# Optimization experiments

Measured on AMD Instinct MI355X. Metric: run time of the kernel, lower is better.

The kernel has to match this reference:

```python
import jax, jax.numpy as jnp
import numpy as np

N = 8192
H = 256
E = N * 32
ALPHA = 0.2  # LeakyReLU negative slope from init kwarg alpha


def setup_inputs() -> dict:
    key = jax.random.key(0)
    ks = jax.random.split(key, 8)
    s = 1.0 / np.sqrt(H)
    return {
        "features": jax.random.normal(ks[0], (N, H), jnp.float32),
        "edge_index": jax.random.randint(ks[1], (2, E), 0, N, jnp.int64),
        "W_att": jax.random.normal(ks[2], (H, H), jnp.float32) * s,
        "a_src": jax.random.normal(ks[3], (H,), jnp.float32) * s,
        "a_dst": jax.random.normal(ks[4], (H,), jnp.float32) * s,
        "gcn_w": jax.random.normal(ks[5], (H, H), jnp.float32) * s,
        "gcn_b": jnp.zeros((H,), jnp.float32),
        "out_w": jax.random.normal(ks[6], (H, 2), jnp.float32) * s,
        "out_b": jnp.zeros((2,), jnp.float32),
    }


def reference(features, edge_index, W_att, a_src, a_dst, gcn_w, gcn_b, out_w, out_b):
    n = features.shape[0]
    # --- SingleNodeAttentionLayer (GAT-style dense self-attention, concat=True) ---
    Wh = features @ W_att                       # [N, H]
    e = jax.nn.leaky_relu(
        (Wh @ a_src)[:, None] + (Wh @ a_dst)[None, :], negative_slope=ALPHA
    )                                            # [N, N]
    attn = jax.nn.softmax(e, axis=-1)
    h1 = jax.nn.elu(attn @ Wh)                   # [N, H]
    # --- GCNConv: symmetric-normalized aggregation with self-loops ---
    loops = jnp.arange(n, dtype=edge_index.dtype)
    row = jnp.concatenate([edge_index[0], loops])  # destination
    col = jnp.concatenate([edge_index[1], loops])  # source
    deg = jax.ops.segment_sum(jnp.ones_like(row, dtype=h1.dtype), row, num_segments=n)
    dinv = jax.lax.rsqrt(jnp.maximum(deg, 1e-12))
    norm = dinv[row] * dinv[col]                 # [E+N]
    x = h1 @ gcn_w                               # [N, H]
    agg = jax.ops.segment_sum(x[col] * norm[:, None], row, num_segments=n) + gcn_b
    # --- head: linear -> mean over nodes -> softmax ---
    res = agg @ out_w + out_b                    # [N, 2]
    res = jnp.mean(res, axis=0, keepdims=True)   # [1, 2]
    return jax.nn.softmax(res, axis=-1)
```

## Files before the change

kernel.cpp:

```cpp
#include <hip/hip_runtime.h>
#include <hip/hip_bf16.h>

#define NN 8192
#define HH 256
#define EE (NN*32)
#define ALPHAC 0.2f
#define CHUNK 16
#define NCHUNK (NN/CHUNK)
#define CSPAD 1024

typedef __bf16 bf16x8 __attribute__((ext_vector_type(8)));
typedef float  f32x4  __attribute__((ext_vector_type(4)));

#define OFF_WH     0
#define OFF_S      (OFF_WH + NN*HH)
#define OFF_D      (OFF_S + NN)
#define OFF_SORTD  (OFF_D + NN)
#define OFF_PERM   (OFF_SORTD + NN)
#define OFF_EA     (OFF_PERM + NN)
#define OFF_E1     (OFF_EA + NN)
#define OFF_SAREL  (OFF_E1 + NN)
#define OFF_SBREL  (OFF_SAREL + NN)
#define OFF_ABPART (OFF_SBREL + NN)
#define OFF_CPAB   (OFF_ABPART + 2*NN*HH)
#define OFF_CSA    (OFF_CPAB + 2*(NCHUNK+1)*HH)
#define OFF_CSB    (OFF_CSA + CSPAD)
#define OFF_DEG    (OFF_CSB + CSPAD)
#define OFF_V      (OFF_DEG + NN)
#define OFF_DINV   (OFF_V + HH)
#define OFF_WNODE  (OFF_DINV + NN)
#define OFF_KEYS   (OFF_WNODE + NN)
#define OFF_FB16   (OFF_KEYS + 2*NN)
#define OFF_WT16   (OFF_FB16 + NN*HH/2)
#define OFF_CNT    (OFF_WT16 + HH*HH/2)
#define OFF_WAS    (OFF_CNT + 16)
#define OFF_WAD    (OFF_WAS + HH)

__device__ __forceinline__ float elu1(float x) {
    return x > 0.f ? x : (expf(x) - 1.f);
}

__global__ __launch_bounds__(256) void k_prep(const float* __restrict__ features,
                                              const float* __restrict__ W_att,
                                              const float* __restrict__ a_src,
                                              const float* __restrict__ a_dst,
                                              float* ws) {
    int bid = blockIdx.x, tid = threadIdx.x;
    int wave = tid >> 6, lane = tid & 63;
    if (bid < 1024) {
        int base = (bid*256 + tid)*8;
        float4 a = *(const float4*)(features + base);
        float4 b = *(const float4*)(features + base + 4);
        bf16x8 v;
        v[0]=(__bf16)a.x; v[1]=(__bf16)a.y; v[2]=(__bf16)a.z; v[3]=(__bf16)a.w;
        v[4]=(__bf16)b.x; v[5]=(__bf16)b.y; v[6]=(__bf16)b.z; v[7]=(__bf16)b.w;
        *(bf16x8*)((__bf16*)(ws + OFF_FB16) + base) = v;
    } else if (bid < 1056) {
        int idx0 = ((bid-1024)*256 + tid)*8;
        __bf16* WT = (__bf16*)(ws + OFF_WT16);
        #pragma unroll
        for (int q = 0; q < 8; ++q) {
            int idx = idx0 + q;
            int n = idx >> 8, k = idx & 255;
            WT[idx] = (__bf16)W_att[(size_t)k*HH + n];
        }
    } else if (bid < 1120) {
        int k = (bid - 1056)*4 + wave;
        float4 w = *(const float4*)(W_att + (size_t)k*HH + lane*4);
        float4 as = *(const float4*)(a_src + lane*4);
        float4 ad = *(const float4*)(a_dst + lane*4);
        float ss = w.x*as.x + w.y*as.y + w.z*as.z + w.w*as.w;
        float dd = w.x*ad.x + w.y*ad.y + w.z*ad.z + w.w*ad.w;
        #pragma unroll
        for (int off = 32; off; off >>= 1) {
            ss += __shfl_xor(ss, off);
            dd += __shfl_xor(dd, off);
        }
        if (lane == 0) {
            ws[OFF_WAS + k] = ss;
            ws[OFF_WAD + k] = dd;
        }
    } else {
        int z0 = ((bid-1120)*256 + tid);
        if (z0 < NN + HH) ws[OFF_DEG + z0] = 0.f;
        if (bid == 1120 && tid < 16) ((unsigned*)(ws + OFF_CNT))[tid] = 0u;
    }
}

__global__ __launch_bounds__(256) void k_gemm_deg_sd(const float* __restrict__ features,
                                                     const int* __restrict__ ei, float* ws) {
    int bid = blockIdx.x, tid = threadIdx.x;
    int wave = tid >> 6, lane = tid & 63;
    if (bid < 512) {
        int mt = bid >> 2, nt = bid & 3;
        int ml = lane & 15, quad = lane >> 4;
        int row0 = mt*64 + wave*16;
        int n0 = nt*64;
        const __bf16* FB = (const __bf16*)(ws + OFF_FB16);
        const __bf16* WT = (const __bf16*)(ws + OFF_WT16);
        const __bf16* Ap = FB + (size_t)(row0 + ml)*HH + quad*8;
        const __bf16* B0 = WT + (size_t)(n0 +  0 + ml)*HH + quad*8;
        const __bf16* B1 = WT + (size_t)(n0 + 16 + ml)*HH + quad*8;
        const __bf16* B2 = WT + (size_t)(n0 + 32 + ml)*HH + quad*8;
        const __bf16* B3 = WT + (size_t)(n0 + 48 + ml)*HH + quad*8;
        f32x4 ac0 = {0.f,0.f,0.f,0.f}, ac1 = ac0, ac2 = ac0, ac3 = ac0;
        #pragma unroll
        for (int k0 = 0; k0 < HH; k0 += 32) {
            bf16x8 af = *(const bf16x8*)(Ap + k0);
            ac0 = __builtin_amdgcn_mfma_f32_16x16x32_bf16(af, *(const bf16x8*)(B0 + k0), ac0, 0, 0, 0);
            ac1 = __builtin_amdgcn_mfma_f32_16x16x32_bf16(af, *(const bf16x8*)(B1 + k0), ac1, 0, 0, 0);
            ac2 = __builtin_amdgcn_mfma_f32_16x16x32_bf16(af, *(const bf16x8*)(B2 + k0), ac2, 0, 0, 0);
            ac3 = __builtin_amdgcn_mfma_f32_16x16x32_bf16(af, *(const bf16x8*)(B3 + k0), ac3, 0, 0, 0);
        }
        float* Whp = ws + OFF_WH;
        #pragma unroll
        for (int r = 0; r < 4; ++r) {
            size_t grow = (size_t)(row0 + quad*4 + r)*HH + n0 + ml;
            Whp[grow +  0] = ac0[r];
            Whp[grow + 16] = ac1[r];
            Whp[grow + 32] = ac2[r];
            Whp[grow + 48] = ac3[r];
        }
    } else {
        int b = bid - 512;
        int e = b*512 + tid;
        atomicAdd(ws + OFF_DEG + ei[e], 1.0f);
        atomicAdd(ws + OFF_DEG + ei[e + 256], 1.0f);
        float4 as = *(const float4*)(ws + OFF_WAS + lane*4);
        float4 ad = *(const float4*)(ws + OFF_WAD + lane*4);
        int row0 = b*16 + wave*4;
        #pragma unroll
        for (int r = 0; r < 4; ++r) {
            int row = row0 + r;
            float4 f = *(const float4*)(features + (size_t)row*HH + lane*4);
            float ss = f.x*as.x + f.y*as.y + f.z*as.z + f.w*as.w;
            float dd = f.x*ad.x + f.y*ad.y + f.z*ad.z + f.w*ad.w;
            #pragma unroll
            for (int off = 32; off; off >>= 1) {
                ss += __shfl_xor(ss, off);
                dd += __shfl_xor(dd, off);
            }
            if (lane == 0) {
                ws[OFF_S+row] = ss; ws[OFF_D+row] = dd;
                unsigned u = __float_as_uint(dd);
                unsigned mono = u ^ ((u & 0x80000000u) ? 0xFFFFFFFFu : 0x80000000u);
                ((unsigned long long*)(ws + OFF_KEYS))[row] =
                    (((unsigned long long)mono) << 13) | (unsigned)row;
            }
        }
    }
}

__global__ __launch_bounds__(256) void k_rank_dinv(float* ws) {
    __shared__ unsigned long long lk[NN];
    int bid = blockIdx.x, tid = threadIdx.x;
    int wave = tid >> 6, lane = tid & 63;
    if (bid < 512) {
        const unsigned long long* keys = (const unsigned long long*)(ws + OFF_KEYS);
        for (int m = tid; m < NN/2; m += 256)
            *(ulonglong2*)&lk[m*2] = *(const ulonglong2*)&keys[m*2];
        __syncthreads();
        int jb = bid*16 + wave*4;
        unsigned long long kj0 = lk[jb+0], kj1 = lk[jb+1];
        unsigned long long kj2 = lk[jb+2], kj3 = lk[jb+3];
        int c0 = 0, c1 = 0, c2 = 0, c3 = 0;
        #pragma unroll 4
        for (int it = 0; it < 64; ++it) {
            ulonglong2 kq = *(const ulonglong2*)&lk[(it*64 + lane)*2];
            c0 += (kq.x < kj0); c1 += (kq.x < kj1);
            c2 += (kq.x < kj2); c3 += (kq.x < kj3);
            c0 += (kq.y < kj0); c1 += (kq.y < kj1);
            c2 += (kq.y < kj2); c3 += (kq.y < kj3);
        }
        #pragma unroll
        for (int off = 1; off < 64; off <<= 1) {
            c0 += __shfl_xor(c0, off);
            c1 += __shfl_xor(c1, off);
            c2 += __shfl_xor(c2, off);
            c3 += __shfl_xor(c3, off);
        }
        if (lane == 0) {
            unsigned long long kk[4] = {kj0, kj1, kj2, kj3};
            int cr[4] = {c0, c1, c2, c3};
            #pragma unroll
            for (int q = 0; q < 4; ++q) {
                unsigned long long kv = kk[q];
                int r = cr[q];
                unsigned mm = (unsigned)(kv >> 13);
                unsigned u = (mm & 0x80000000u) ? (mm ^ 0x80000000u) : ~mm;
                float dj = __uint_as_float(u);
                int j = (int)(kv & 8191ULL);
                ws[OFF_SORTD + r] = dj;
                ((int*)ws)[OFF_PERM + r] = j;
                ws[OFF_EA + r] = expf(ALPHAC * dj);
                ws[OFF_E1 + r] = expf(dj);
            }
        }
    } else {
        int i = (bid - 512)*256 + tid;
        float dv = rsqrtf(ws[OFF_DEG + i] + 1.0f);
        ws[OFF_DINV + i] = dv;
        ws[OFF_WNODE + i] = dv*dv;
    }
}

__global__ __launch_bounds__(256) void k_wnode_vecpref(const int* __restrict__ ei, float* ws) {
    int bid = blockIdx.x, tid = threadIdx.x;
    if (bid < NCHUNK) {
        __shared__ int   sp[CHUNK];
        __shared__ float sea[CHUNK], se1[CHUNK];
        int c = bid, h = tid;
        int k0 = c * CHUNK;
        if (h < CHUNK) {
            sp[h]  = ((int*)ws)[OFF_PERM + k0 + h];
            sea[h] = ws[OFF_EA + k0 + h];
            se1[h] = ws[OFF_E1 + k0 + h];
        }
        __syncthreads();
        if (tid < 64) {
            int lane = tid;
            float v = 0.f;
            if (lane < 16) v = sea[lane];
            else if (lane < 32) v = se1[lane-16];
            #pragma unroll
            for (int off = 1; off < 16; off <<= 1) {
                float x = __shfl_up(v, off);
                if ((lane & 15) >= off) v += x;
            }
            if (lane < 16) {
                ws[OFF_SAREL + k0 + lane] = v;
                if (lane == 15) ws[OFF_CSA + c + 1] = v;
            } else if (lane < 32) {
                ws[OFF_SBREL + k0 + lane - 16] = v;
                if (lane == 31) ws[OFF_CSB + c + 1] = v;
            }
        }
        const float* Wh = ws + OFF_WH;
        float wv[CHUNK];
        #pragma unroll
        for (int kk = 0; kk < CHUNK; ++kk)
            wv[kk] = Wh[(size_t)sp[kk]*HH + h];
        float2* abp = (float2*)(ws + OFF_ABPART);
        float acca = 0.f, accb = 0.f;
        #pragma unroll
        for (int kk = 0; kk < CHUNK; ++kk) {
            acca += sea[kk]*wv[kk]; accb += se1[kk]*wv[kk];
            abp[(size_t)(k0+kk)*HH + h] = make_float2(acca, accb);
        }
        float2* cp = (float2*)(ws + OFF_CPAB);
        cp[(size_t)(c+1)*HH + h] = make_float2(acca, accb);
    } else {
        int e = (bid - NCHUNK)*512 + tid;
        int r0 = ei[e],       c0i = ei[EE + e];
        int r1 = ei[e + 256], c1i = ei[EE + e + 256];
        atomicAdd(ws + OFF_WNODE + c0i, ws[OFF_DINV + r0] * ws[OFF_DINV + c0i]);
        atomicAdd(ws + OFF_WNODE + c1i, ws[OFF_DINV + r1] * ws[OFF_DINV + c1i]);
    }
}

__global__ __launch_bounds__(256) void k_chunkscan(float* ws) {
    int bid = blockIdx.x, tid = threadIdx.x;
    if (bid < 32) {
        int h = bid*8 + (tid >> 5);
        int t = tid & 31;
        float2* cp = (float2*)(ws + OFF_CPAB);
        float la[16], lb[16];
        float ta = 0.f, tb = 0.f;
        #pragma unroll
        for (int m = 0; m < 16; ++m) {
            float2 v = cp[(size_t)(t*16 + m + 1)*HH + h];
            la[m] = v.x; lb[m] = v.y;
            ta += la[m]; tb += lb[m];
        }
        float ia = ta, ib = tb;
        #pragma unroll
        for (int off = 1; off < 32; off <<= 1) {
            float xa = __shfl_up(ia, off, 32);
            float xb = __shfl_up(ib, off, 32);
            if (t >= off) { ia += xa; ib += xb; }
        }
        float ba = ia - ta, bb = ib - tb;
        #pragma unroll
        for (int m = 0; m < 16; ++m) {
            cp[(size_t)(t*16 + m)*HH + h] = make_float2(ba, bb);
            ba += la[m]; bb += lb[m];
        }
        if (t == 31) cp[(size_t)NCHUNK*HH + h] = make_float2(ba, bb);
    } else {
        int lane = tid & 63, wvi = tid >> 6;
        bool act = wvi < 2;
        float* cs = ws + (wvi == 1 ? OFF_CSB : OFF_CSA);
        float la[8];
        float ta = 0.f;
        if (act) {
            #pragma unroll
            for (int m = 0; m < 8; ++m) { la[m] = cs[lane*8 + m + 1]; ta += la[m]; }
        }
        float ia = ta;
        #pragma unroll
        for (int off = 1; off < 64; off <<= 1) {
            float x = __shfl_up(ia, off);
            if (lane >= off) ia += x;
        }
        float ba = ia - ta;
        __syncthreads();
        if (act) {
            #pragma unroll
            for (int m = 0; m < 8; ++m) { cs[lane*8 + m] = ba; ba += la[m]; }
            if (lane == 63) cs[NCHUNK] = ba;
        }
    }
}

__global__ __launch_bounds__(256) void k_rows_final(
        const float* __restrict__ gcn_w, const float* __restrict__ gcn_b,
        const float* __restrict__ out_w, const float* __restrict__ out_b,
        float* ws, float* out) {
    __shared__ float sd[NN];
    __shared__ float red[4][256];
    __shared__ float fin[768];
    __shared__ int islast;
    int tid = threadIdx.x;
    for (int m = tid; m < NN/4; m += 256)
        *(float4*)&sd[m*4] = *(const float4*)(ws + OFF_SORTD + m*4);
    __syncthreads();
    int wave = tid >> 6, lane = tid & 63;
    int gw = blockIdx.x*4 + wave;
    const float2* abp  = (const float2*)(ws + OFF_ABPART);
    const float2* cpab = (const float2*)(ws + OFF_CPAB);
    float btot = ws[OFF_CSB + NCHUNK];
    const float4* btr = (const float4*)(cpab + (size_t)NCHUNK*HH);
    float4 bt0 = btr[lane*2], bt1 = btr[lane*2+1];
    float BTx = bt0.y, BTy = bt0.w, BTz = bt1.y, BTw = bt1.w;

    int myr = lane & 3;
    float si_m = ws[OFF_S + gw*4 + myr];
    float tt = -si_m;
    int lo = 0, hi = NN;
    while (lo < hi) {
        int mid = (lo + hi) >> 1;
        if (sd[mid] <= tt) lo = mid + 1; else hi = mid;
    }

    float accx = 0.f, accy = 0.f, accz = 0.f, accw = 0.f;
    #pragma unroll
    for (int r = 0; r < 4; ++r) {
        int i = gw*4 + r;
        int k = __shfl(lo, r);
        float si = __shfl(si_m, r);
        float eas = expf(ALPHAC * si), es = expf(si);
        float av = 0.f, bv = 0.f;
        float Ax=0.f, Ay=0.f, Az=0.f, Aw=0.f, Bx=0.f, By=0.f, Bz=0.f, Bw=0.f;
        if (k > 0) {
            int km = k - 1, cc = km >> 4;
            av = ws[OFF_CSA + cc] + ws[OFF_SAREL + km];
            bv = ws[OFF_CSB + cc] + ws[OFF_SBREL + km];
            const float4* pr = (const float4*)(abp + (size_t)km*HH);
            const float4* cr = (const float4*)(cpab + (size_t)cc*HH);
            float4 p0 = pr[lane*2], p1 = pr[lane*2+1];
            float4 q0 = cr[lane*2], q1 = cr[lane*2+1];
            Ax = p0.x + q0.x; Bx = p0.y + q0.y;
            Ay = p0.z + q0.z; By = p0.w + q0.w;
            Az = p1.x + q1.x; Bz = p1.y + q1.y;
            Aw = p1.z + q1.z; Bw = p1.w + q1.w;
        }
        float Z = eas*av + es*(btot - bv);
        float invZ = 1.f / Z;
        float w = ws[OFF_WNODE + i];
        accx += w * elu1((eas*Ax + es*(BTx - Bx)) * invZ);
        accy += w * elu1((eas*Ay + es*(BTy - By)) * invZ);
        accz += w * elu1((eas*Az + es*(BTz - Bz)) * invZ);
        accw += w * elu1((eas*Aw + es*(BTw - Bw)) * invZ);
    }
    red[wave][lane*4+0] = accx;
    red[wave][lane*4+1] = accy;
    red[wave][lane*4+2] = accz;
    red[wave][lane*4+3] = accw;
    __syncthreads();
    float sum = red[0][tid] + red[1][tid] + red[2][tid] + red[3][tid];
    atomicAdd(ws + OFF_V + tid, sum);

    __syncthreads();
    if (tid == 0) {
        unsigned* cnt = (unsigned*)(ws + OFF_CNT);
        unsigned arrived = __hip_atomic_fetch_add(&cnt[0], 1u,
                               __ATOMIC_ACQ_REL, __HIP_MEMORY_SCOPE_AGENT) + 1u;
        islast = (arrived == 512u);
    }
    __syncthreads();
    if (islast) {
        float* vl  = fin;
        float* r0s = fin + 256;
        float* r1s = fin + 512;
        int t = tid;
        vl[t] = __hip_atomic_load(ws + OFF_V + t, __ATOMIC_RELAXED,
                                  __HIP_MEMORY_SCOPE_AGENT);
        __syncthreads();
        float acc = 0.f;
        for (int h = 0; h < HH; ++h) acc += vl[h] * gcn_w[(size_t)h*HH + t];
        float meanv = acc * (1.0f/(float)NN) + gcn_b[t];
        r0s[t] = meanv * out_w[t*2+0];
        r1s[t] = meanv * out_w[t*2+1];
        __syncthreads();
        for (int off = 128; off; off >>= 1) {
            if (t < off) { r0s[t] += r0s[t+off]; r1s[t] += r1s[t+off]; }
            __syncthreads();
        }
        if (t == 0) {
            float res0 = r0s[0] + out_b[0], res1 = r1s[0] + out_b[1];
            float m = fmaxf(res0, res1);
            float e0 = expf(res0 - m), e1v = expf(res1 - m);
            float inv = 1.f / (e0 + e1v);
            out[0] = e0 * inv;
            out[1] = e1v * inv;
        }
    }
}

extern "C" void kernel_launch(void* const* d_in, const int* in_sizes, int n_in,
                              void* d_out, int out_size, void* d_ws, size_t ws_size,
                              hipStream_t stream) {
    const float* features = (const float*)d_in[0];
    const int*   eidx     = (const int*)d_in[1];
    const float* W_att    = (const float*)d_in[2];
    const float* a_src    = (const float*)d_in[3];
    const float* a_dst    = (const float*)d_in[4];
    const float* gcn_w    = (const float*)d_in[5];
    const float* gcn_b    = (const float*)d_in[6];
    const float* out_w    = (const float*)d_in[7];
    const float* out_b    = (const float*)d_in[8];
    float* ws  = (float*)d_ws;
    float* out = (float*)d_out;

    k_prep<<<1154, 256, 0, stream>>>(features, W_att, a_src, a_dst, ws);
    k_gemm_deg_sd<<<1024, 256, 0, stream>>>(features, eidx, ws);
    k_rank_dinv<<<544, 256, 0, stream>>>(ws);
    k_wnode_vecpref<<<1024, 256, 0, stream>>>(eidx, ws);
    k_chunkscan<<<33, 256, 0, stream>>>(ws);
    k_rows_final<<<NN/16, 256, 0, stream>>>(gcn_w, gcn_b, out_w, out_b, ws, out);
}
```

Baseline: 163.1 us.

## Fuse bf16 feature conversion into GEMM and rank 32-bit keys from global

Drops the separate features-to-bf16 pass in the prep kernel. The GEMM now loads fp32 features directly and converts them in registers, which removes a full 8 MB write plus read-back of the bf16 copy and shrinks the prep launch. The rank kernel now compares 32-bit monotone keys read straight from global memory, breaking ties by index, instead of staging 64-bit packed keys into 64 KB of LDS. That lowers LDS use and raises occupancy, at the cost of more global/L2 reads per block and extra compare work per element.

```diff
diff --git a/kernel.cpp b/kernel.cpp
--- a/kernel.cpp
+++ b/kernel.cpp
@@ -30,8 +30,7 @@
 #define OFF_DINV   (OFF_V + HH)
 #define OFF_WNODE  (OFF_DINV + NN)
 #define OFF_KEYS   (OFF_WNODE + NN)
-#define OFF_FB16   (OFF_KEYS + 2*NN)
-#define OFF_WT16   (OFF_FB16 + NN*HH/2)
+#define OFF_WT16   (OFF_KEYS + NN)
 #define OFF_CNT    (OFF_WT16 + HH*HH/2)
 #define OFF_WAS    (OFF_CNT + 16)
 #define OFF_WAD    (OFF_WAS + HH)
@@ -40,23 +39,14 @@
     return x > 0.f ? x : (expf(x) - 1.f);
 }
 
-__global__ __launch_bounds__(256) void k_prep(const float* __restrict__ features,
-                                              const float* __restrict__ W_att,
+__global__ __launch_bounds__(256) void k_prep(const float* __restrict__ W_att,
                                               const float* __restrict__ a_src,
                                               const float* __restrict__ a_dst,
                                               float* ws) {
     int bid = blockIdx.x, tid = threadIdx.x;
     int wave = tid >> 6, lane = tid & 63;
-    if (bid < 1024) {
-        int base = (bid*256 + tid)*8;
-        float4 a = *(const float4*)(features + base);
-        float4 b = *(const float4*)(features + base + 4);
-        bf16x8 v;
-        v[0]=(__bf16)a.x; v[1]=(__bf16)a.y; v[2]=(__bf16)a.z; v[3]=(__bf16)a.w;
-        v[4]=(__bf16)b.x; v[5]=(__bf16)b.y; v[6]=(__bf16)b.z; v[7]=(__bf16)b.w;
-        *(bf16x8*)((__bf16*)(ws + OFF_FB16) + base) = v;
-    } else if (bid < 1056) {
-        int idx0 = ((bid-1024)*256 + tid)*8;
+    if (bid < 32) {
+        int idx0 = (bid*256 + tid)*8;
         __bf16* WT = (__bf16*)(ws + OFF_WT16);
         #pragma unroll
         for (int q = 0; q < 8; ++q) {
@@ -64,8 +54,8 @@
             int n = idx >> 8, k = idx & 255;
             WT[idx] = (__bf16)W_att[(size_t)k*HH + n];
         }
-    } else if (bid < 1120) {
-        int k = (bid - 1056)*4 + wave;
+    } else if (bid < 96) {
+        int k = (bid - 32)*4 + wave;
         float4 w = *(const float4*)(W_att + (size_t)k*HH + lane*4);
         float4 as = *(const float4*)(a_src + lane*4);
         float4 ad = *(const float4*)(a_dst + lane*4);
@@ -81,9 +71,9 @@
             ws[OFF_WAD + k] = dd;
         }
     } else {
-        int z0 = ((bid-1120)*256 + tid);
+        int z0 = ((bid-96)*256 + tid);
         if (z0 < NN + HH) ws[OFF_DEG + z0] = 0.f;
-        if (bid == 1120 && tid < 16) ((unsigned*)(ws + OFF_CNT))[tid] = 0u;
+        if (bid == 96 && tid < 16) ((unsigned*)(ws + OFF_CNT))[tid] = 0u;
     }
 }
 
@@ -96,9 +86,8 @@
         int ml = lane & 15, quad = lane >> 4;
         int row0 = mt*64 + wave*16;
         int n0 = nt*64;
-        const __bf16* FB = (const __bf16*)(ws + OFF_FB16);
+        const float*  Ap = features + (size_t)(row0 + ml)*HH + quad*8;
         const __bf16* WT = (const __bf16*)(ws + OFF_WT16);
-        const __bf16* Ap = FB + (size_t)(row0 + ml)*HH + quad*8;
         const __bf16* B0 = WT + (size_t)(n0 +  0 + ml)*HH + quad*8;
         const __bf16* B1 = WT + (size_t)(n0 + 16 + ml)*HH + quad*8;
         const __bf16* B2 = WT + (size_t)(n0 + 32 + ml)*HH + quad*8;
@@ -106,7 +95,11 @@
         f32x4 ac0 = {0.f,0.f,0.f,0.f}, ac1 = ac0, ac2 = ac0, ac3 = ac0;
         #pragma unroll
         for (int k0 = 0; k0 < HH; k0 += 32) {
-            bf16x8 af = *(const bf16x8*)(Ap + k0);
+            float4 fa = *(const float4*)(Ap + k0);
+            float4 fb = *(const float4*)(Ap + k0 + 4);
+            bf16x8 af;
+            af[0]=(__bf16)fa.x; af[1]=(__bf16)fa.y; af[2]=(__bf16)fa.z; af[3]=(__bf16)fa.w;
+            af[4]=(__bf16)fb.x; af[5]=(__bf16)fb.y; af[6]=(__bf16)fb.z; af[7]=(__bf16)fb.w;
             ac0 = __builtin_amdgcn_mfma_f32_16x16x32_bf16(af, *(const bf16x8*)(B0 + k0), ac0, 0, 0, 0);
             ac1 = __builtin_amdgcn_mfma_f32_16x16x32_bf16(af, *(const bf16x8*)(B1 + k0), ac1, 0, 0, 0);
             ac2 = __builtin_amdgcn_mfma_f32_16x16x32_bf16(af, *(const bf16x8*)(B2 + k0), ac2, 0, 0, 0);
@@ -144,33 +137,41 @@
                 ws[OFF_S+row] = ss; ws[OFF_D+row] = dd;
                 unsigned u = __float_as_uint(dd);
                 unsigned mono = u ^ ((u & 0x80000000u) ? 0xFFFFFFFFu : 0x80000000u);
-                ((unsigned long long*)(ws + OFF_KEYS))[row] =
-                    (((unsigned long long)mono) << 13) | (unsigned)row;
+                ((unsigned*)(ws + OFF_KEYS))[row] = mono;
             }
         }
     }
 }
 
 __global__ __launch_bounds__(256) void k_rank_dinv(float* ws) {
-    __shared__ unsigned long long lk[NN];
     int bid = blockIdx.x, tid = threadIdx.x;
     int wave = tid >> 6, lane = tid & 63;
     if (bid < 512) {
-        const unsigned long long* keys = (const unsigned long long*)(ws + OFF_KEYS);
-        for (int m = tid; m < NN/2; m += 256)
-            *(ulonglong2*)&lk[m*2] = *(const ulonglong2*)&keys[m*2];
-        __syncthreads();
-        int jb = bid*16 + wave*4;
-        unsigned long long kj0 = lk[jb+0], kj1 = lk[jb+1];
-        unsigned long long kj2 = lk[jb+2], kj3 = lk[jb+3];
+        const unsigned* km = (const unsigned*)(ws + OFF_KEYS);
+        int i0 = bid*16 + wave*4;
+        unsigned mi0 = km[i0+0], mi1 = km[i0+1];
+        unsigned mi2 = km[i0+2], mi3 = km[i0+3];
         int c0 = 0, c1 = 0, c2 = 0, c3 = 0;
         #pragma unroll 4
-        for (int it = 0; it < 64; ++it) {
-            ulonglong2 kq = *(const ulonglong2*)&lk[(it*64 + lane)*2];
-            c0 += (kq.x < kj0); c1 += (kq.x < kj1);
-            c2 += (kq.x < kj2); c3 += (kq.x < kj3);
-            c0 += (kq.y < kj0); c1 += (kq.y < kj1);
-            c2 += (kq.y < kj2); c3 += (kq.y < kj3);
+        for (int it = 0; it < 32; ++it) {
+            int j = it*256 + lane*4;
+            uint4 kq = *(const uint4*)(km + j);
+            c0 += (kq.x < mi0) + ((kq.x == mi0) & (j+0 < i0+0));
+            c1 += (kq.x < mi1) + ((kq.x == mi1) & (j+0 < i0+1));
+            c2 += (kq.x < mi2) + ((kq.x == mi2) & (j+0 < i0+2));
+            c3 += (kq.x < mi3) + ((kq.x == mi3) & (j+0 < i0+3));
+            c0 += (kq.y < mi0) + ((kq.y == mi0) & (j+1 < i0+0));
+            c1 += (kq.y < mi1) + ((kq.y == mi1) & (j+1 < i0+1));
+            c2 += (kq.y < mi2) + ((kq.y == mi2) & (j+1 < i0+2));
+            c3 += (kq.y < mi3) + ((kq.y == mi3) & (j+1 < i0+3));
+            c0 += (kq.z < mi0) + ((kq.z == mi0) & (j+2 < i0+0));
+            c1 += (kq.z < mi1) + ((kq.z == mi1) & (j+2 < i0+1));
+            c2 += (kq.z < mi2) + ((kq.z == mi2) & (j+2 < i0+2));
+            c3 += (kq.z < mi3) + ((kq.z == mi3) & (j+2 < i0+3));
+            c0 += (kq.w < mi0) + ((kq.w == mi0) & (j+3 < i0+0));
+            c1 += (kq.w < mi1) + ((kq.w == mi1) & (j+3 < i0+1));
+            c2 += (kq.w < mi2) + ((kq.w == mi2) & (j+3 < i0+2));
+            c3 += (kq.w < mi3) + ((kq.w == mi3) & (j+3 < i0+3));
         }
         #pragma unroll
         for (int off = 1; off < 64; off <<= 1) {
@@ -180,18 +181,16 @@
             c3 += __shfl_xor(c3, off);
         }
         if (lane == 0) {
-            unsigned long long kk[4] = {kj0, kj1, kj2, kj3};
+            unsigned mm[4] = {mi0, mi1, mi2, mi3};
             int cr[4] = {c0, c1, c2, c3};
             #pragma unroll
             for (int q = 0; q < 4; ++q) {
-                unsigned long long kv = kk[q];
                 int r = cr[q];
-                unsigned mm = (unsigned)(kv >> 13);
-                unsigned u = (mm & 0x80000000u) ? (mm ^ 0x80000000u) : ~mm;
+                unsigned m = mm[q];
+                unsigned u = (m & 0x80000000u) ? (m ^ 0x80000000u) : ~m;
                 float dj = __uint_as_float(u);
-                int j = (int)(kv & 8191ULL);
                 ws[OFF_SORTD + r] = dj;
-                ((int*)ws)[OFF_PERM + r] = j;
+                ((int*)ws)[OFF_PERM + r] = i0 + q;
                 ws[OFF_EA + r] = expf(ALPHAC * dj);
                 ws[OFF_E1 + r] = expf(dj);
             }
@@ -432,7 +431,7 @@
     float* ws  = (float*)d_ws;
     float* out = (float*)d_out;
 
-    k_prep<<<1154, 256, 0, stream>>>(features, W_att, a_src, a_dst, ws);
+    k_prep<<<130, 256, 0, stream>>>(W_att, a_src, a_dst, ws);
     k_gemm_deg_sd<<<1024, 256, 0, stream>>>(features, eidx, ws);
     k_rank_dinv<<<544, 256, 0, stream>>>(ws);
     k_wnode_vecpref<<<1024, 256, 0, stream>>>(eidx, ws);
```

After: 164.4 us. No clear change (+0.8%).
